# Optimization experiments

Hardware: AMD Instinct MI355X
Metric: run time of the kernel (lower is better)

Reference implementation:

```python
import jax, jax.numpy as jnp
import numpy as np

WIN = 7          # window_size
DIM = 192        # embedding dim
HEADS = 6
HEAD_DIM = DIM // HEADS
B_ = 4096        # batch * num_windows
N = WIN * WIN    # tokens per window


def _relative_position_index():
    coords = np.stack(np.meshgrid(np.arange(WIN), np.arange(WIN), indexing='ij'))  # [2,7,7]
    flat = coords.reshape(2, -1)                                                   # [2,49]
    rel = flat[:, :, None] - flat[:, None, :]                                      # [2,49,49]
    rel = rel.transpose(1, 2, 0).astype(np.int32)                                  # [49,49,2]
    rel[:, :, 0] += WIN - 1
    rel[:, :, 1] += WIN - 1
    rel[:, :, 0] *= 2 * WIN - 1
    return jnp.asarray(rel.sum(-1), dtype=jnp.int32)                               # [49,49]


def setup_inputs() -> dict:
    key = jax.random.key(0)
    ks = jax.random.split(key, 6)
    std = 0.02
    return {
        'x': jax.random.normal(ks[0], (B_, N, DIM), dtype=jnp.float32),
        'qkv_w': jax.random.normal(ks[1], (3 * DIM, DIM), dtype=jnp.float32) * std,
        'qkv_b': jnp.zeros((3 * DIM,), dtype=jnp.float32),
        'proj_w': jax.random.normal(ks[2], (DIM, DIM), dtype=jnp.float32) * std,
        'proj_b': jnp.zeros((DIM,), dtype=jnp.float32),
        'bias_table': jax.random.normal(ks[3], ((2 * WIN - 1) ** 2, HEADS), dtype=jnp.float32) * std,
        'rel_index': _relative_position_index(),
    }


def reference(x, qkv_w, qkv_b, proj_w, proj_b, bias_table, rel_index):
    B, n, C = x.shape
    # qkv projection -> [3, B, H, N, hd]
    qkv = (x @ qkv_w.T + qkv_b).reshape(B, n, 3, HEADS, HEAD_DIM)
    qkv = jnp.transpose(qkv, (2, 0, 3, 1, 4))
    q, k, v = qkv[0], qkv[1], qkv[2]
    # relative position bias: [H, N, N]
    bias = bias_table[rel_index.reshape(-1)].reshape(n, n, HEADS)
    bias = jnp.transpose(bias, (2, 0, 1))[None]  # [1, H, N, N]
    scale = 1.0 / jnp.sqrt(jnp.asarray(HEAD_DIM, dtype=x.dtype))
    logits = jnp.einsum('bhnd,bhmd->bhnm', q, k) * scale + bias
    attn = jax.nn.softmax(logits, axis=-1)
    out = jnp.einsum('bhnm,bhmd->bhnd', attn, v)
    out = jnp.transpose(out, (0, 2, 1, 3)).reshape(B, n, C)
    return out @ proj_w.T + proj_b
```

## Files before the change

kernel.cpp:

```cpp
#include <hip/hip_runtime.h>

#define NTOK 49
#define DIM 192
#define HEADS 6

typedef __bf16 bf16x8 __attribute__((ext_vector_type(8)));
typedef float f32x4 __attribute__((ext_vector_type(4)));

#define WPROJ_USH 110592
#define BIAS_BYTE 294912

#define SCALE 0.17677669529663687f

#define OUT_WIN_BYTES 37632

__device__ __forceinline__ unsigned int pack2(float a, float b) {
    unsigned short lo = __builtin_bit_cast(unsigned short, (__bf16)a);
    unsigned short hi = __builtin_bit_cast(unsigned short, (__bf16)b);
    return (unsigned int)lo | ((unsigned int)hi << 16);
}

__device__ __forceinline__ f32x4 mfma16(int4 a, int4 b, f32x4 c) {
    return __builtin_amdgcn_mfma_f32_16x16x32_bf16(
        __builtin_bit_cast(bf16x8, a), __builtin_bit_cast(bf16x8, b), c, 0, 0, 0);
}

__global__ void prep(const float* __restrict__ qkv_w, const float* __restrict__ proj_w,
                     const float* __restrict__ bias_table, const int* __restrict__ rel_index,
                     unsigned short* __restrict__ w16, float* __restrict__ bias_cd) {
    int bid = blockIdx.x;
    if (bid < 72) {
        int c = bid * 256 + threadIdx.x;
        const float* src; unsigned short* dst; int OT; int cc; int isq = 0;
        if (c < 13824)      { src = qkv_w;  dst = w16;             OT = 36; cc = c; isq = 1; }
        else                { src = proj_w; dst = w16 + WPROJ_USH; OT = 12; cc = c - 13824; }
        int lane = cc & 63;
        int t = cc >> 6;
        int ot = t % OT, ks = t / OT;
        int f  = ot * 16 + (lane & 15);
        int k0 = ks * 32 + (lane >> 4) * 8;
        float sc = (isq && f < 192) ? SCALE : 1.0f;
        const float* p = src + (size_t)f * DIM + k0;
        float4 a = *(const float4*)p;
        float4 b = *(const float4*)(p + 4);
        uint4 o;
        o.x = pack2(a.x * sc, a.y * sc); o.y = pack2(a.z * sc, a.w * sc);
        o.z = pack2(b.x * sc, b.y * sc); o.w = pack2(b.z * sc, b.w * sc);
        *(uint4*)(dst + (size_t)cc * 8) = o;
    } else {
        int gid = (bid - 72) * 256 + threadIdx.x;
        int lane = gid & 63;
        int tile = (gid >> 6) & 15;
        int h    = gid >> 10;
        int kt = tile >> 2, qt = tile & 3;
        int qtok = qt * 16 + (lane & 15);
        int key0 = kt * 16 + (lane >> 4) * 4;
        float4 v;
        float* vp = (float*)&v;
        for (int r = 0; r < 4; ++r) {
            int key = key0 + r;
            float val;
            if (key >= NTOK)       val = -1e30f;
            else if (qtok >= NTOK) val = 0.0f;
            else                   val = bias_table[rel_index[qtok * NTOK + key] * HEADS + h];
            vp[r] = val;
        }
        *(float4*)(bias_cd + (size_t)gid * 4) = v;
    }
}

#define SCR_OFF 24576
#define K1_LDS 27648

__global__ __launch_bounds__(192, 2) void win_attn(
    const float* __restrict__ x,
    const float* __restrict__ qkv_b,
    const unsigned short* __restrict__ wq16,
    const float* __restrict__ bias_cd,
    float* __restrict__ outO)
{
    extern __shared__ char smem[];
    const int tid  = threadIdx.x;
    const int lane = tid & 63;
    const int wv   = tid >> 6;
    const int widx = blockIdx.x;
    const int l15  = lane & 15;
    const int quad = lane >> 4;

    #pragma unroll
    for (int i = 0; i < 8; ++i) {
        int c  = tid + i * 192;
        int cl = c & 63;
        int mt = (c >> 6) & 3;
        int ks = c >> 8;
        int tok = mt * 16 + (cl & 15);
        int d0  = ks * 32 + (cl >> 4) * 8;
        uint4 o = {0u, 0u, 0u, 0u};
        if (tok < NTOK) {
            const float* p = x + ((size_t)widx * NTOK + tok) * DIM + d0;
            float4 a  = *(const float4*)p;
            float4 bb = *(const float4*)(p + 4);
            o.x = pack2(a.x, a.y); o.y = pack2(a.z, a.w);
            o.z = pack2(bb.x, bb.y); o.w = pack2(bb.z, bb.w);
        }
        *(uint4*)(smem + (size_t)c * 16) = o;
    }
    __syncthreads();

    char* const xrd = smem + lane * 16;
    char* const buf = smem + SCR_OFF + wv * 1024;
    char* const swr = buf + (quad & 1) * 8 + l15 * 16 + (quad >> 1) * 256;
    char* const srd = buf + lane * 16;

    #pragma unroll 1
    for (int hi = 0; hi < 2; ++hi) {
        const int h = wv + hi * 3;
        const unsigned short* const wqh = wq16 + (size_t)(h * 128 + lane) * 8;
        const float* const bcb = bias_cd + (size_t)(h * 1024 + lane) * 4;

        int4 qf[4];
        {
            f32x4 qa[2][4];
            #pragma unroll
            for (int ft = 0; ft < 2; ++ft)
                #pragma unroll
                for (int nt = 0; nt < 4; ++nt) qa[ft][nt] = (f32x4){0,0,0,0};
            #pragma unroll 2
            for (int ks = 0; ks < 6; ++ks) {
                int4 wq[2];
                #pragma unroll
                for (int ft = 0; ft < 2; ++ft)
                    wq[ft] = *(const int4*)(wqh + (ks*36 + ft) * 512);
                #pragma unroll
                for (int nt = 0; nt < 4; ++nt) {
                    int4 xf = *(const int4*)(xrd + (ks*4 + nt) * 1024);
                    #pragma unroll
                    for (int ft = 0; ft < 2; ++ft)
                        qa[ft][nt] = mfma16(wq[ft], xf, qa[ft][nt]);
                }
            }
            float4 bq[2];
            #pragma unroll
            for (int ft = 0; ft < 2; ++ft) {
                float4 t = *(const float4*)(qkv_b + (h*2 + ft)*16 + quad*4);
                bq[ft].x = t.x*SCALE; bq[ft].y = t.y*SCALE; bq[ft].z = t.z*SCALE; bq[ft].w = t.w*SCALE;
            }
            #pragma unroll
            for (int nt = 0; nt < 4; ++nt) {
                #pragma unroll
                for (int ft = 0; ft < 2; ++ft) {
                    uint2 w;
                    w.x = pack2(qa[ft][nt][0] + bq[ft].x, qa[ft][nt][1] + bq[ft].y);
                    w.y = pack2(qa[ft][nt][2] + bq[ft].z, qa[ft][nt][3] + bq[ft].w);
                    *(uint2*)(swr + ft * 512) = w;
                }
                qf[nt] = *(const int4*)srd;
            }
        }

        int4 kf[4];
        {
            f32x4 ka[2][4];
            #pragma unroll
            for (int ft = 0; ft < 2; ++ft)
                #pragma unroll
                for (int nt = 0; nt < 4; ++nt) ka[ft][nt] = (f32x4){0,0,0,0};
            #pragma unroll 2
            for (int ks = 0; ks < 6; ++ks) {
                int4 wk[2];
                #pragma unroll
                for (int ft = 0; ft < 2; ++ft)
                    wk[ft] = *(const int4*)(wqh + (ks*36 + ft) * 512 + 6144);
                #pragma unroll
                for (int nt = 0; nt < 4; ++nt) {
                    int4 xf = *(const int4*)(xrd + (ks*4 + nt) * 1024);
                    #pragma unroll
                    for (int ft = 0; ft < 2; ++ft)
                        ka[ft][nt] = mfma16(wk[ft], xf, ka[ft][nt]);
                }
            }
            float4 bk[2];
            #pragma unroll
            for (int ft = 0; ft < 2; ++ft)
                bk[ft] = *(const float4*)(qkv_b + 192 + (h*2 + ft)*16 + quad*4);
            #pragma unroll
            for (int nt = 0; nt < 4; ++nt) {
                #pragma unroll
                for (int ft = 0; ft < 2; ++ft) {
                    uint2 w;
                    w.x = pack2(ka[ft][nt][0] + bk[ft].x, ka[ft][nt][1] + bk[ft].y);
                    w.y = pack2(ka[ft][nt][2] + bk[ft].z, ka[ft][nt][3] + bk[ft].w);
                    *(uint2*)(swr + ft * 512) = w;
                }
                kf[nt] = *(const int4*)srd;
            }
        }

        float inv[4];
        int4 pf[2][4];
        #pragma unroll
        for (int qt = 0; qt < 4; ++qt) {
            float sum = 0.f;
            #pragma unroll
            for (int ksn = 0; ksn < 2; ++ksn) {
                #pragma unroll
                for (int kt2 = 0; kt2 < 2; ++kt2) {
                    const int kt = ksn*2 + kt2;
                    f32x4 z = {0,0,0,0};
                    f32x4 s = mfma16(kf[kt], qf[qt], z);
                    float4 bc = *(const float4*)(bcb + (kt*4 + qt) * 256);
                    float e0 = __expf(s[0] + bc.x);
                    float e1 = __expf(s[1] + bc.y);
                    float e2 = __expf(s[2] + bc.z);
                    float e3 = __expf(s[3] + bc.w);
                    sum += (e0 + e1) + (e2 + e3);
                    uint2 w;
                    w.x = pack2(e0, e1);
                    w.y = pack2(e2, e3);
                    *(uint2*)(swr + kt2 * 512) = w;
                }
                pf[ksn][qt] = *(const int4*)srd;
            }
            sum += __shfl_xor(sum, 16);
            sum += __shfl_xor(sum, 32);
            inv[qt] = 1.0f / sum;
        }

        int4 vf[2][2];
        {
            f32x4 va[4][2];
            #pragma unroll
            for (int mt = 0; mt < 4; ++mt)
                #pragma unroll
                for (int nv = 0; nv < 2; ++nv) va[mt][nv] = (f32x4){0,0,0,0};
            #pragma unroll 2
            for (int ks = 0; ks < 6; ++ks) {
                int4 wvv[2];
                #pragma unroll
                for (int nv = 0; nv < 2; ++nv)
                    wvv[nv] = *(const int4*)(wqh + (ks*36 + nv) * 512 + 12288);
                #pragma unroll
                for (int mt = 0; mt < 4; ++mt) {
                    int4 xf = *(const int4*)(xrd + (ks*4 + mt) * 1024);
                    #pragma unroll
                    for (int nv = 0; nv < 2; ++nv)
                        va[mt][nv] = mfma16(xf, wvv[nv], va[mt][nv]);
                }
            }
            const float bv0 = qkv_b[384 + h*32 + l15];
            const float bv1 = qkv_b[384 + h*32 + 16 + l15];
            #pragma unroll
            for (int ksn = 0; ksn < 2; ++ksn) {
                #pragma unroll
                for (int nv = 0; nv < 2; ++nv) {
                    const float bv = nv ? bv1 : bv0;
                    #pragma unroll
                    for (int mt2 = 0; mt2 < 2; ++mt2) {
                        const int mt = ksn*2 + mt2;
                        uint2 w;
                        w.x = pack2(va[mt][nv][0] + bv, va[mt][nv][1] + bv);
                        w.y = pack2(va[mt][nv][2] + bv, va[mt][nv][3] + bv);
                        *(uint2*)(swr + mt2 * 512) = w;
                    }
                    vf[ksn][nv] = *(const int4*)srd;
                }
            }
        }

        f32x4 oacc[2][4];
        #pragma unroll
        for (int dmt = 0; dmt < 2; ++dmt)
            #pragma unroll
            for (int qt = 0; qt < 4; ++qt) oacc[dmt][qt] = (f32x4){0, 0, 0, 0};
        #pragma unroll
        for (int ksn = 0; ksn < 2; ++ksn)
            #pragma unroll
            for (int dmt = 0; dmt < 2; ++dmt)
                #pragma unroll
                for (int qt = 0; qt < 4; ++qt)
                    oacc[dmt][qt] = mfma16(vf[ksn][dmt], pf[ksn][qt], oacc[dmt][qt]);

        char* const og = (char*)outO + (size_t)widx * OUT_WIN_BYTES + (size_t)(h * 4) * 1024;
        #pragma unroll
        for (int qt = 0; qt < 4; ++qt) {
            uint2 w0, w1;
            w0.x = pack2(oacc[0][qt][0] * inv[qt], oacc[0][qt][1] * inv[qt]);
            w0.y = pack2(oacc[0][qt][2] * inv[qt], oacc[0][qt][3] * inv[qt]);
            *(uint2*)(swr + 0) = w0;
            w1.x = pack2(oacc[1][qt][0] * inv[qt], oacc[1][qt][1] * inv[qt]);
            w1.y = pack2(oacc[1][qt][2] * inv[qt], oacc[1][qt][3] * inv[qt]);
            *(uint2*)(swr + 512) = w1;
            int4 line = *(const int4*)srd;
            *(int4*)(og + qt * 1024 + lane * 16) = line;
        }
    }
}

#define K2_LDS 24576

__global__ __launch_bounds__(384, 4) void proj_k(
    float* __restrict__ out,
    const unsigned short* __restrict__ wp16,
    const float* __restrict__ proj_b)
{
    extern __shared__ char smem[];
    const int tid  = threadIdx.x;
    const int lane = tid & 63;
    const int h    = tid >> 6;
    const int l15  = lane & 15;
    const int quad = lane >> 4;
    const int widx = blockIdx.x;

    char* const base = (char*)out + (size_t)widx * OUT_WIN_BYTES;
    #pragma unroll
    for (int i = 0; i < 4; ++i) {
        int c = tid + i * 384;
        *(uint4*)(smem + (size_t)c * 16) = *(const uint4*)(base + (size_t)c * 16);
    }
    __syncthreads();

    char* const xrd = smem + lane * 16;
    const unsigned short* const wph = wp16 + (size_t)(h * 128 + lane) * 8;

    f32x4 acc[4][2];
    #pragma unroll
    for (int mt = 0; mt < 4; ++mt)
        #pragma unroll
        for (int j = 0; j < 2; ++j) acc[mt][j] = (f32x4){0, 0, 0, 0};
    #pragma unroll 2
    for (int ks = 0; ks < 6; ++ks) {
        int4 wb[2];
        #pragma unroll
        for (int j = 0; j < 2; ++j)
            wb[j] = *(const int4*)(wph + (ks*12 + j) * 512);
        #pragma unroll
        for (int mt = 0; mt < 4; ++mt) {
            int4 oa = *(const int4*)(xrd + (ks*4 + mt) * 1024);
            #pragma unroll
            for (int j = 0; j < 2; ++j)
                acc[mt][j] = mfma16(oa, wb[j], acc[mt][j]);
        }
    }
    #pragma unroll
    for (int j = 0; j < 2; ++j) {
        const int o = (h*2 + j) * 16 + l15;
        const float pb = proj_b[o];
        #pragma unroll
        for (int mt = 0; mt < 4; ++mt) {
            const int t0 = mt * 16 + quad * 4;
            #pragma unroll
            for (int r = 0; r < 4; ++r) {
                const int t = t0 + r;
                if (t < NTOK)
                    out[((size_t)widx * NTOK + t) * DIM + o] = acc[mt][j][r] + pb;
            }
        }
    }
}

extern "C" void kernel_launch(void* const* d_in, const int* in_sizes, int n_in,
                              void* d_out, int out_size, void* d_ws, size_t ws_size,
                              hipStream_t stream) {
    const float* x          = (const float*)d_in[0];
    const float* qkv_w      = (const float*)d_in[1];
    const float* qkv_b      = (const float*)d_in[2];
    const float* proj_w     = (const float*)d_in[3];
    const float* proj_b     = (const float*)d_in[4];
    const float* bias_table = (const float*)d_in[5];
    const int*   rel_index  = (const int*)d_in[6];
    float* out = (float*)d_out;

    unsigned short* w16 = (unsigned short*)d_ws;
    float* bias_cd = (float*)((char*)d_ws + BIAS_BYTE);

    prep<<<96, 256, 0, stream>>>(qkv_w, proj_w, bias_table, rel_index, w16, bias_cd);

    (void)hipFuncSetAttribute((const void*)win_attn,
                              hipFuncAttributeMaxDynamicSharedMemorySize, K1_LDS);
    win_attn<<<4096, 192, K1_LDS, stream>>>(x, qkv_b, w16, bias_cd, out);

    (void)hipFuncSetAttribute((const void*)proj_k,
                              hipFuncAttributeMaxDynamicSharedMemorySize, K2_LDS);
    proj_k<<<4096, 384, K2_LDS, stream>>>(out, w16 + WPROJ_USH, proj_b);
}
```

Before: 393.3 us.

## Use 16x16x16 bf16 MFMA to keep attention operands in registers

Switches the QK^T, PV and output-projection matmuls to the 16x16x16 bf16 MFMA, whose accumulator layout matches the operand layout the next MFMA expects. Q, K, V and the probability fragments can then be packed straight from registers, with no round trip through LDS scratch, and the per-head LDS scratch region is dropped. The Q and K projections are merged into one loop. The attention output is now written in a 16-wide k-slice layout that proj_k reads directly, and the proj weight prep is rewritten to match. The cost is twice as many half-size MFMAs in the attention and projection stages, plus higher register pressure from holding Q and K accumulators together.

After: 398.8 us. Within noise of the previous version (+1.4%).

```diff
diff --git a/kernel.cpp b/kernel.cpp
--- a/kernel.cpp
+++ b/kernel.cpp
@@ -6,6 +6,8 @@
 
 typedef __bf16 bf16x8 __attribute__((ext_vector_type(8)));
 typedef float f32x4 __attribute__((ext_vector_type(4)));
+typedef unsigned int u32x2 __attribute__((ext_vector_type(2)));
+typedef short s16x4 __attribute__((ext_vector_type(4)));
 
 #define WPROJ_USH 110592
 #define BIAS_BYTE 294912
@@ -20,10 +22,27 @@
     return (unsigned int)lo | ((unsigned int)hi << 16);
 }
 
-__device__ __forceinline__ f32x4 mfma16(int4 a, int4 b, f32x4 c) {
+__device__ __forceinline__ f32x4 mfma32(int4 a, int4 b, f32x4 c) {
     return __builtin_amdgcn_mfma_f32_16x16x32_bf16(
         __builtin_bit_cast(bf16x8, a), __builtin_bit_cast(bf16x8, b), c, 0, 0, 0);
 }
+
+#if __has_builtin(__builtin_amdgcn_mfma_f32_16x16x16bf16_1k)
+__device__ __forceinline__ f32x4 mfma16(u32x2 a, u32x2 b, f32x4 c) {
+    return __builtin_amdgcn_mfma_f32_16x16x16bf16_1k(
+        __builtin_bit_cast(s16x4, a), __builtin_bit_cast(s16x4, b), c, 0, 0, 0);
+}
+#else
+__device__ __forceinline__ f32x4 mfma16(u32x2 a, u32x2 b, f32x4 c) {
+    f32x4 d;
+    asm volatile("s_nop 1\n\t"
+                 "v_mfma_f32_16x16x16_bf16 %0, %1, %2, %3\n\t"
+                 "s_nop 7\n\t"
+                 "s_nop 7"
+                 : "=v"(d) : "v"(a), "v"(b), "0"(c));
+    return d;
+}
+#endif
 
 __global__ void prep(const float* __restrict__ qkv_w, const float* __restrict__ proj_w,
                      const float* __restrict__ bias_table, const int* __restrict__ rel_index,
@@ -31,22 +50,38 @@
     int bid = blockIdx.x;
     if (bid < 72) {
         int c = bid * 256 + threadIdx.x;
-        const float* src; unsigned short* dst; int OT; int cc; int isq = 0;
-        if (c < 13824)      { src = qkv_w;  dst = w16;             OT = 36; cc = c; isq = 1; }
-        else                { src = proj_w; dst = w16 + WPROJ_USH; OT = 12; cc = c - 13824; }
-        int lane = cc & 63;
-        int t = cc >> 6;
-        int ot = t % OT, ks = t / OT;
-        int f  = ot * 16 + (lane & 15);
-        int k0 = ks * 32 + (lane >> 4) * 8;
-        float sc = (isq && f < 192) ? SCALE : 1.0f;
-        const float* p = src + (size_t)f * DIM + k0;
-        float4 a = *(const float4*)p;
-        float4 b = *(const float4*)(p + 4);
-        uint4 o;
-        o.x = pack2(a.x * sc, a.y * sc); o.y = pack2(a.z * sc, a.w * sc);
-        o.z = pack2(b.x * sc, b.y * sc); o.w = pack2(b.z * sc, b.w * sc);
-        *(uint4*)(dst + (size_t)cc * 8) = o;
+        if (c < 13824) {
+            int lane = c & 63;
+            int t = c >> 6;
+            int ot = t % 36, ks = t / 36;
+            int f  = ot * 16 + (lane & 15);
+            int k0 = ks * 32 + (lane >> 4) * 8;
+            float sc = (f < 192) ? SCALE : 1.0f;
+            const float* p = qkv_w + (size_t)f * DIM + k0;
+            float4 a = *(const float4*)p;
+            float4 b = *(const float4*)(p + 4);
+            uint4 o;
+            o.x = pack2(a.x * sc, a.y * sc); o.y = pack2(a.z * sc, a.w * sc);
+            o.z = pack2(b.x * sc, b.y * sc); o.w = pack2(b.z * sc, b.w * sc);
+            *(uint4*)(w16 + (size_t)c * 8) = o;
+        } else {
+            int cc = c - 13824;
+            int line = cc >> 5;
+            int pair = cc & 31;
+            int ks = line / 12, ot = line % 12;
+            unsigned int w[4];
+            #pragma unroll
+            for (int s = 0; s < 2; ++s) {
+                int lane = pair * 2 + s;
+                int q = lane >> 4, ci = lane & 15;
+                const float* p = proj_w + (size_t)(ot*16 + ci) * DIM + ks*16 + q*4;
+                float4 a = *(const float4*)p;
+                w[s*2 + 0] = pack2(a.x, a.y);
+                w[s*2 + 1] = pack2(a.z, a.w);
+            }
+            uint4 o = {w[0], w[1], w[2], w[3]};
+            *(uint4*)(w16 + WPROJ_USH + (size_t)cc * 8) = o;
+        }
     } else {
         int gid = (bid - 72) * 256 + threadIdx.x;
         int lane = gid & 63;
@@ -69,8 +104,7 @@
     }
 }
 
-#define SCR_OFF 24576
-#define K1_LDS 27648
+#define K1_LDS 24576
 
 __global__ __launch_bounds__(192, 2) void win_attn(
     const float* __restrict__ x,
@@ -108,9 +142,6 @@
     __syncthreads();
 
     char* const xrd = smem + lane * 16;
-    char* const buf = smem + SCR_OFF + wv * 1024;
-    char* const swr = buf + (quad & 1) * 8 + l15 * 16 + (quad >> 1) * 256;
-    char* const srd = buf + lane * 16;
 
     #pragma unroll 1
     for (int hi = 0; hi < 2; ++hi) {
@@ -118,115 +149,69 @@
         const unsigned short* const wqh = wq16 + (size_t)(h * 128 + lane) * 8;
         const float* const bcb = bias_cd + (size_t)(h * 1024 + lane) * 4;
 
-        int4 qf[4];
+        u32x2 qb[2][4], kb[2][4];
         {
-            f32x4 qa[2][4];
+            f32x4 qa[2][4], ka[2][4];
             #pragma unroll
             for (int ft = 0; ft < 2; ++ft)
                 #pragma unroll
-                for (int nt = 0; nt < 4; ++nt) qa[ft][nt] = (f32x4){0,0,0,0};
+                for (int nt = 0; nt < 4; ++nt) { qa[ft][nt] = (f32x4){0,0,0,0}; ka[ft][nt] = (f32x4){0,0,0,0}; }
             #pragma unroll 2
             for (int ks = 0; ks < 6; ++ks) {
-                int4 wq[2];
-                #pragma unroll
-                for (int ft = 0; ft < 2; ++ft)
+                int4 wq[2], wk[2];
+                #pragma unroll
+                for (int ft = 0; ft < 2; ++ft) {
                     wq[ft] = *(const int4*)(wqh + (ks*36 + ft) * 512);
+                    wk[ft] = *(const int4*)(wqh + (ks*36 + ft) * 512 + 6144);
+                }
                 #pragma unroll
                 for (int nt = 0; nt < 4; ++nt) {
                     int4 xf = *(const int4*)(xrd + (ks*4 + nt) * 1024);
                     #pragma unroll
-                    for (int ft = 0; ft < 2; ++ft)
-                        qa[ft][nt] = mfma16(wq[ft], xf, qa[ft][nt]);
+                    for (int ft = 0; ft < 2; ++ft) {
+                        qa[ft][nt] = mfma32(wq[ft], xf, qa[ft][nt]);
+                        ka[ft][nt] = mfma32(wk[ft], xf, ka[ft][nt]);
+                    }
                 }
             }
-            float4 bq[2];
             #pragma unroll
             for (int ft = 0; ft < 2; ++ft) {
-                float4 t = *(const float4*)(qkv_b + (h*2 + ft)*16 + quad*4);
-                bq[ft].x = t.x*SCALE; bq[ft].y = t.y*SCALE; bq[ft].z = t.z*SCALE; bq[ft].w = t.w*SCALE;
-            }
-            #pragma unroll
-            for (int nt = 0; nt < 4; ++nt) {
-                #pragma unroll
-                for (int ft = 0; ft < 2; ++ft) {
-                    uint2 w;
-                    w.x = pack2(qa[ft][nt][0] + bq[ft].x, qa[ft][nt][1] + bq[ft].y);
-                    w.y = pack2(qa[ft][nt][2] + bq[ft].z, qa[ft][nt][3] + bq[ft].w);
-                    *(uint2*)(swr + ft * 512) = w;
+                float4 tq = *(const float4*)(qkv_b + (h*2 + ft)*16 + quad*4);
+                float4 tk = *(const float4*)(qkv_b + 192 + (h*2 + ft)*16 + quad*4);
+                #pragma unroll
+                for (int nt = 0; nt < 4; ++nt) {
+                    qb[ft][nt] = (u32x2){ pack2(qa[ft][nt][0] + tq.x*SCALE, qa[ft][nt][1] + tq.y*SCALE),
+                                          pack2(qa[ft][nt][2] + tq.z*SCALE, qa[ft][nt][3] + tq.w*SCALE) };
+                    kb[ft][nt] = (u32x2){ pack2(ka[ft][nt][0] + tk.x, ka[ft][nt][1] + tk.y),
+                                          pack2(ka[ft][nt][2] + tk.z, ka[ft][nt][3] + tk.w) };
                 }
-                qf[nt] = *(const int4*)srd;
-            }
-        }
-
-        int4 kf[4];
-        {
-            f32x4 ka[2][4];
-            #pragma unroll
-            for (int ft = 0; ft < 2; ++ft)
-                #pragma unroll
-                for (int nt = 0; nt < 4; ++nt) ka[ft][nt] = (f32x4){0,0,0,0};
-            #pragma unroll 2
-            for (int ks = 0; ks < 6; ++ks) {
-                int4 wk[2];
-                #pragma unroll
-                for (int ft = 0; ft < 2; ++ft)
-                    wk[ft] = *(const int4*)(wqh + (ks*36 + ft) * 512 + 6144);
-                #pragma unroll
-                for (int nt = 0; nt < 4; ++nt) {
-                    int4 xf = *(const int4*)(xrd + (ks*4 + nt) * 1024);
-                    #pragma unroll
-                    for (int ft = 0; ft < 2; ++ft)
-                        ka[ft][nt] = mfma16(wk[ft], xf, ka[ft][nt]);
-                }
-            }
-            float4 bk[2];
-            #pragma unroll
-            for (int ft = 0; ft < 2; ++ft)
-                bk[ft] = *(const float4*)(qkv_b + 192 + (h*2 + ft)*16 + quad*4);
-            #pragma unroll
-            for (int nt = 0; nt < 4; ++nt) {
-                #pragma unroll
-                for (int ft = 0; ft < 2; ++ft) {
-                    uint2 w;
-                    w.x = pack2(ka[ft][nt][0] + bk[ft].x, ka[ft][nt][1] + bk[ft].y);
-                    w.y = pack2(ka[ft][nt][2] + bk[ft].z, ka[ft][nt][3] + bk[ft].w);
-                    *(uint2*)(swr + ft * 512) = w;
-                }
-                kf[nt] = *(const int4*)srd;
             }
         }
 
         float inv[4];
-        int4 pf[2][4];
+        u32x2 pf[4][4];
         #pragma unroll
         for (int qt = 0; qt < 4; ++qt) {
             float sum = 0.f;
             #pragma unroll
-            for (int ksn = 0; ksn < 2; ++ksn) {
-                #pragma unroll
-                for (int kt2 = 0; kt2 < 2; ++kt2) {
-                    const int kt = ksn*2 + kt2;
-                    f32x4 z = {0,0,0,0};
-                    f32x4 s = mfma16(kf[kt], qf[qt], z);
-                    float4 bc = *(const float4*)(bcb + (kt*4 + qt) * 256);
-                    float e0 = __expf(s[0] + bc.x);
-                    float e1 = __expf(s[1] + bc.y);
-                    float e2 = __expf(s[2] + bc.z);
-                    float e3 = __expf(s[3] + bc.w);
-                    sum += (e0 + e1) + (e2 + e3);
-                    uint2 w;
-                    w.x = pack2(e0, e1);
-                    w.y = pack2(e2, e3);
-                    *(uint2*)(swr + kt2 * 512) = w;
-                }
-                pf[ksn][qt] = *(const int4*)srd;
+            for (int kt = 0; kt < 4; ++kt) {
+                f32x4 s = (f32x4){0,0,0,0};
+                s = mfma16(kb[0][kt], qb[0][qt], s);
+                s = mfma16(kb[1][kt], qb[1][qt], s);
+                float4 bc = *(const float4*)(bcb + (kt*4 + qt) * 256);
+                float e0 = __expf(s[0] + bc.x);
+                float e1 = __expf(s[1] + bc.y);
+                float e2 = __expf(s[2] + bc.z);
+                float e3 = __expf(s[3] + bc.w);
+                sum += (e0 + e1) + (e2 + e3);
+                pf[kt][qt] = (u32x2){ pack2(e0, e1), pack2(e2, e3) };
             }
             sum += __shfl_xor(sum, 16);
             sum += __shfl_xor(sum, 32);
             inv[qt] = 1.0f / sum;
         }
 
-        int4 vf[2][2];
+        u32x2 vb[4][2];
         {
             f32x4 va[4][2];
             #pragma unroll
@@ -244,54 +229,42 @@
                     int4 xf = *(const int4*)(xrd + (ks*4 + mt) * 1024);
                     #pragma unroll
                     for (int nv = 0; nv < 2; ++nv)
-                        va[mt][nv] = mfma16(xf, wvv[nv], va[mt][nv]);
+                        va[mt][nv] = mfma32(xf, wvv[nv], va[mt][nv]);
                 }
             }
             const float bv0 = qkv_b[384 + h*32 + l15];
             const float bv1 = qkv_b[384 + h*32 + 16 + l15];
             #pragma unroll
-            for (int ksn = 0; ksn < 2; ++ksn) {
-                #pragma unroll
-                for (int nv = 0; nv < 2; ++nv) {
-                    const float bv = nv ? bv1 : bv0;
-                    #pragma unroll
-                    for (int mt2 = 0; mt2 < 2; ++mt2) {
-                        const int mt = ksn*2 + mt2;
-                        uint2 w;
-                        w.x = pack2(va[mt][nv][0] + bv, va[mt][nv][1] + bv);
-                        w.y = pack2(va[mt][nv][2] + bv, va[mt][nv][3] + bv);
-                        *(uint2*)(swr + mt2 * 512) = w;
-                    }
-                    vf[ksn][nv] = *(const int4*)srd;
-                }
+            for (int mt = 0; mt < 4; ++mt) {
+                vb[mt][0] = (u32x2){ pack2(va[mt][0][0] + bv0, va[mt][0][1] + bv0),
+                                     pack2(va[mt][0][2] + bv0, va[mt][0][3] + bv0) };
+                vb[mt][1] = (u32x2){ pack2(va[mt][1][0] + bv1, va[mt][1][1] + bv1),
+                                     pack2(va[mt][1][2] + bv1, va[mt][1][3] + bv1) };
             }
         }
 
         f32x4 oacc[2][4];
         #pragma unroll
-        for (int dmt = 0; dmt < 2; ++dmt)
-            #pragma unroll
-            for (int qt = 0; qt < 4; ++qt) oacc[dmt][qt] = (f32x4){0, 0, 0, 0};
-        #pragma unroll
-        for (int ksn = 0; ksn < 2; ++ksn)
-            #pragma unroll
-            for (int dmt = 0; dmt < 2; ++dmt)
+        for (int nv = 0; nv < 2; ++nv)
+            #pragma unroll
+            for (int qt = 0; qt < 4; ++qt) oacc[nv][qt] = (f32x4){0,0,0,0};
+        #pragma unroll
+        for (int mt = 0; mt < 4; ++mt)
+            #pragma unroll
+            for (int nv = 0; nv < 2; ++nv)
                 #pragma unroll
                 for (int qt = 0; qt < 4; ++qt)
-                    oacc[dmt][qt] = mfma16(vf[ksn][dmt], pf[ksn][qt], oacc[dmt][qt]);
-
-        char* const og = (char*)outO + (size_t)widx * OUT_WIN_BYTES + (size_t)(h * 4) * 1024;
-        #pragma unroll
-        for (int qt = 0; qt < 4; ++qt) {
-            uint2 w0, w1;
-            w0.x = pack2(oacc[0][qt][0] * inv[qt], oacc[0][qt][1] * inv[qt]);
-            w0.y = pack2(oacc[0][qt][2] * inv[qt], oacc[0][qt][3] * inv[qt]);
-            *(uint2*)(swr + 0) = w0;
-            w1.x = pack2(oacc[1][qt][0] * inv[qt], oacc[1][qt][1] * inv[qt]);
-            w1.y = pack2(oacc[1][qt][2] * inv[qt], oacc[1][qt][3] * inv[qt]);
-            *(uint2*)(swr + 512) = w1;
-            int4 line = *(const int4*)srd;
-            *(int4*)(og + qt * 1024 + lane * 16) = line;
+                    oacc[nv][qt] = mfma16(vb[mt][nv], pf[mt][qt], oacc[nv][qt]);
+
+        char* const og = (char*)outO + (size_t)widx * OUT_WIN_BYTES;
+        #pragma unroll
+        for (int nv = 0; nv < 2; ++nv) {
+            #pragma unroll
+            for (int qt = 0; qt < 4; ++qt) {
+                u32x2 ow = (u32x2){ pack2(oacc[nv][qt][0] * inv[qt], oacc[nv][qt][1] * inv[qt]),
+                                    pack2(oacc[nv][qt][2] * inv[qt], oacc[nv][qt][3] * inv[qt]) };
+                *(u32x2*)(og + (size_t)(((h*2 + nv)*4 + qt) * 512) + lane * 8) = ow;
+            }
         }
     }
 }
@@ -319,23 +292,23 @@
     }
     __syncthreads();
 
-    char* const xrd = smem + lane * 16;
-    const unsigned short* const wph = wp16 + (size_t)(h * 128 + lane) * 8;
+    char* const ard = smem + lane * 8;
+    const char* const wpb = (const char*)wp16 + lane * 8;
 
     f32x4 acc[4][2];
     #pragma unroll
     for (int mt = 0; mt < 4; ++mt)
         #pragma unroll
         for (int j = 0; j < 2; ++j) acc[mt][j] = (f32x4){0, 0, 0, 0};
-    #pragma unroll 2
-    for (int ks = 0; ks < 6; ++ks) {
-        int4 wb[2];
+    #pragma unroll 3
+    for (int ks = 0; ks < 12; ++ks) {
+        u32x2 wb[2];
         #pragma unroll
         for (int j = 0; j < 2; ++j)
-            wb[j] = *(const int4*)(wph + (ks*12 + j) * 512);
+            wb[j] = *(const u32x2*)(wpb + (size_t)((ks*12 + h*2 + j) * 512));
         #pragma unroll
         for (int mt = 0; mt < 4; ++mt) {
-            int4 oa = *(const int4*)(xrd + (ks*4 + mt) * 1024);
+            u32x2 oa = *(const u32x2*)(ard + (ks*4 + mt) * 512);
             #pragma unroll
             for (int j = 0; j < 2; ++j)
                 acc[mt][j] = mfma16(oa, wb[j], acc[mt][j]);
```
